# Kernel optimization log

Hardware: AMD Instinct MI355X
Metric: run time of the kernel (lower is better)

Reference implementation:

```python
import jax, jax.numpy as jnp
import numpy as np

# Model dims (scaled-down ModelArgs, ratios preserved)
B, L, Dm = 2, 1024, 1024
H, KVH = 16, 4
HD = Dm // H          # head_dim = 64
N = 64                # ssm_state_dim
E, TOPK = 4, 2        # num_experts, expert_top_k
FF = 4 * Dm           # expert hidden
ROUTER_MIX = np.array([0.5, 0.2, 0.15, 0.15], dtype=np.float32)  # layer_idx=0 -> ssm-heavy


def _rms(x, w, eps=1e-6):
    return x * jax.lax.rsqrt(jnp.mean(x * x, axis=-1, keepdims=True) + eps) * w


def setup_inputs() -> dict:
    key = jax.random.key(0)
    ks = jax.random.split(key, 32)
    f32 = jnp.float32
    def nrm(k, shape, s=0.02):
        return (s * jax.random.normal(k, shape)).astype(f32)
    inp = {
        'x': jax.random.normal(ks[0], (B, L, Dm), dtype=f32),
        'goal_cond': 0.1 * jax.random.normal(ks[1], (B, L, Dm), dtype=f32),
        'mem_out': jax.random.normal(ks[2], (B, L, Dm), dtype=f32),
        'norm1_w': jnp.ones((Dm,), f32),
        'norm2_w': jnp.ones((Dm,), f32),
        'router_w': nrm(ks[3], (Dm, 4)),
        'xproj_w': nrm(ks[4], (Dm, 2 * N + H)),
        'A': (-1.0 + 0.1 * jax.random.normal(ks[5], (H, N))).astype(f32),
        'Dp': jnp.ones((H,), f32),
        'gate_w': nrm(ks[6], (Dm, Dm)),
        'gate_b': jnp.zeros((Dm,), f32),
        'ssd_o_w': nrm(ks[7], (Dm, Dm)),
        'q_w': nrm(ks[8], (Dm, Dm)),
        'k_w': nrm(ks[9], (Dm, KVH * HD)),
        'v_w': nrm(ks[10], (Dm, KVH * HD)),
        'o_w': nrm(ks[11], (Dm, Dm)),
        'qn_w': jnp.ones((HD,), f32),
        'kn_w': jnp.ones((HD,), f32),
        'dw_w': nrm(ks[12], (Dm, 3), 0.3),
        'dw_b': jnp.zeros((Dm,), f32),
        'pw_w': nrm(ks[13], (Dm, Dm)),
        'pw_b': jnp.zeros((Dm,), f32),
        'moe_gate_w': nrm(ks[14], (Dm, E)),
        'e_w1': nrm(ks[15], (E, Dm, 2 * FF)),
        'e_w2': nrm(ks[16], (E, FF, Dm)),
        'e_lin_w': nrm(ks[17], (E, Dm, Dm)),
        'e_lin_b': jnp.zeros((E, Dm), f32),
    }
    return inp


def reference(x, goal_cond, mem_out, norm1_w, norm2_w, router_w, xproj_w, A, Dp,
              gate_w, gate_b, ssd_o_w, q_w, k_w, v_w, o_w, qn_w, kn_w,
              dw_w, dw_b, pw_w, pw_b, moe_gate_w, e_w1, e_w2, e_lin_w, e_lin_b):
    b, l, d = x.shape
    res = x
    xn = _rms(x, norm1_w) + goal_cond

    # --- router over 4 paths ---
    w = jax.nn.softmax(xn @ router_w, axis=-1) * jnp.asarray(ROUTER_MIX, x.dtype)
    w = w / w.sum(axis=-1, keepdims=True)  # [B,L,4]

    # --- SSD (Mamba-2 style selective scan) ---
    ssm = xn @ xproj_w                              # [B,L,2N+H]
    Bs, Cs, db = ssm[..., :N], ssm[..., N:2 * N], ssm[..., 2 * N:]
    delta = jax.nn.softplus(db[..., None] + Bs[..., None, :])   # [B,L,H,N]

    def step(s, dt):                                 # s,dt: [B,H,N]
        s = jnp.exp(dt * A) * s + dt * dt
        return s, s
    _, states = jax.lax.scan(step, jnp.zeros((b, H, N), x.dtype), jnp.moveaxis(delta, 1, 0))
    states = jnp.moveaxis(states, 0, 1)              # [B,L,H,N]
    y = jnp.einsum('blhn,bln->blh', states, Cs)      # contract state dim with C
    xg = xn.reshape(b, l, H, HD)
    y = (y[..., None] + xg * Dp[:, None]).reshape(b, l, d)
    gate = jax.nn.sigmoid(xn @ gate_w + gate_b)
    out_ssd = (y * gate) @ ssd_o_w

    # --- GQA attention with qk-norm + RoPE ---
    q = (xn @ q_w).reshape(b, l, H, HD).transpose(0, 2, 1, 3)      # [B,H,L,hd]
    k = (xn @ k_w).reshape(b, l, KVH, HD).transpose(0, 2, 1, 3)
    v = (xn @ v_w).reshape(b, l, KVH, HD).transpose(0, 2, 1, 3)
    q, k = _rms(q, qn_w), _rms(k, kn_w)
    inv_freq = 1.0 / (10000.0 ** (jnp.arange(0, HD, 2, dtype=jnp.float32) / HD))
    fr = jnp.arange(l, dtype=jnp.float32)[:, None] * inv_freq[None, :]
    emb = jnp.concatenate([fr, fr], axis=-1)
    cos, sin = jnp.cos(emb).astype(x.dtype), jnp.sin(emb).astype(x.dtype)
    def rot(u):
        u1, u2 = jnp.split(u, 2, axis=-1)
        return jnp.concatenate([-u2, u1], axis=-1)
    q = q * cos + rot(q) * sin
    k = k * cos + rot(k) * sin
    k = jnp.repeat(k, H // KVH, axis=1)
    v = jnp.repeat(v, H // KVH, axis=1)
    sc = jnp.einsum('bhqd,bhkd->bhqk', q, k) / jnp.sqrt(jnp.asarray(HD, x.dtype))
    attn = jnp.einsum('bhqk,bhkd->bhqd', jax.nn.softmax(sc, axis=-1), v)
    out_attn = attn.transpose(0, 2, 1, 3).reshape(b, l, d) @ o_w

    # --- depthwise conv3 -> silu -> pointwise conv1 ---
    xp = jnp.pad(xn, ((0, 0), (1, 1), (0, 0)))
    dw = xp[:, :-2] * dw_w[:, 0] + xp[:, 1:-1] * dw_w[:, 1] + xp[:, 2:] * dw_w[:, 2] + dw_b
    out_conv = jax.nn.silu(dw) @ pw_w + pw_b

    mixed = (w[..., 0:1] * out_ssd + w[..., 1:2] * out_attn +
             w[..., 2:3] * out_conv + w[..., 3:4] * mem_out)
    x2 = res + mixed

    # --- dense top-k MoE (experts applied over full x as in source) ---
    gp = jax.nn.softmax(_rms(x2, norm2_w) @ moe_gate_w, axis=-1)     # [B,L,E]
    topp, topi = jax.lax.top_k(gp, TOPK)
    wfull = (jax.nn.one_hot(topi, E, dtype=x.dtype) * topp[..., None]).sum(axis=-2)  # [B,L,E]
    moe = jnp.zeros_like(x2)
    for e in range(E):
        h = x2 @ e_w1[e]                     # [B,L,2*FF]
        a, g = jnp.split(h, 2, axis=-1)
        h = (jax.nn.silu(a) * g) @ e_w2[e]   # [B,L,D]
        eo = h @ e_lin_w[e] + e_lin_b[e]
        moe = moe + wfull[..., e:e + 1] * eo
    return x2 + moe
```

## Files before the change

### kernel.cpp

```cpp
#include <hip/hip_runtime.h>
#include <hip/hip_bf16.h>
#include <cstdint>

typedef unsigned short u16;
typedef __attribute__((ext_vector_type(4))) float f32x4;
typedef __attribute__((ext_vector_type(8))) short s16x8;

#define DEV __device__ __forceinline__

DEV u16 f2bf(float x) {
  unsigned u = __float_as_uint(x);
  u += 0x7FFFu + ((u >> 16) & 1u);
  return (u16)(u >> 16);
}
DEV float bf2f(u16 b) { return __uint_as_float(((unsigned)b) << 16); }

DEV void gload16(const void* g, void* l) {
  __builtin_amdgcn_global_load_lds(
      (const __attribute__((address_space(1))) void*)g,
      (__attribute__((address_space(3))) void*)l, 16, 0, 0);
}

template<bool MAXOP>
DEV float blockRed256(float v) {
  for (int o = 32; o; o >>= 1) {
    float t = __shfl_xor(v, o);
    v = MAXOP ? fmaxf(v, t) : v + t;
  }
  __shared__ float s[4];
  __syncthreads();
  if ((threadIdx.x & 63) == 0) s[threadIdx.x >> 6] = v;
  __syncthreads();
  return MAXOP ? fmaxf(fmaxf(s[0], s[1]), fmaxf(s[2], s[3]))
               : (s[0] + s[1] + s[2] + s[3]);
}

struct WtB { const float* in[8]; u16* out[8]; };
__global__ __launch_bounds__(256) void wtransb_k(WtB wb, int K, int N, int ilv) {
  const float* __restrict__ in = wb.in[blockIdx.z];
  u16* __restrict__ out = wb.out[blockIdx.z];
  __shared__ float t[64][68];
  const int n0 = blockIdx.x * 64, k0 = blockIdx.y * 64;
  const int tt = threadIdx.x;
  const int kl = tt >> 4, nl = (tt & 15) * 4;
#pragma unroll
  for (int i = 0; i < 4; ++i) {
    int k = kl + i * 16;
    float4 v{0.f, 0.f, 0.f, 0.f};
    if (n0 + nl + 3 < N) {
      v = *(const float4*)(in + (long long)(k0 + k) * N + n0 + nl);
    } else {
      for (int j = 0; j < 4; ++j)
        if (n0 + nl + j < N) ((float*)&v)[j] = in[(long long)(k0 + k) * N + n0 + nl + j];
    }
    t[nl + 0][k] = v.x; t[nl + 1][k] = v.y; t[nl + 2][k] = v.z; t[nl + 3][k] = v.w;
  }
  __syncthreads();
  const int n = tt >> 2, kq = (tt & 3) * 16;
  if (n0 + n < N) {
    s16x8 o0, o1;
#pragma unroll
    for (int j = 0; j < 8; ++j) { o0[j] = (short)f2bf(t[n][kq + j]); o1[j] = (short)f2bf(t[n][kq + 8 + j]); }
    int c = n0 + n;
    int r = ilv ? ((((c & 4095) >> 4) << 5) + ((c >> 12) << 4) + (c & 15)) : c;
    u16* op = out + (long long)r * K + k0 + kq;
    *(s16x8*)op = o0; *(s16x8*)(op + 8) = o1;
  }
}

struct GemmP {
  const u16* A; int lda; long long sAz;
  const u16* B; int ldb; long long sBz;
  void* C; int ldc; long long sCz;
  int M, N, K;
  int gqa;
  int czmode;
  const float *p0, *p1, *p2, *p3;
  float scale; int eidx;
  u16 *aux0, *aux1, *aux2;
  const int* cnt;
  const int* s2t;
  int xcdr;
};

template<int EPI, int TN>
__global__ __launch_bounds__(256) void gemm_k(GemmP p) {
  constexpr int NF = TN / 32;
  __shared__ u16 Al[2][128 * 64];
  __shared__ u16 Bl[2][TN * 64];
  __shared__ float sminv[128];
  int bx = blockIdx.x, by = blockIdx.y, z = blockIdx.z;
  if (p.xcdr) {
    const int nx = gridDim.x, ny = gridDim.y;
    const int chunk = nx >> 3;
    int flat = (blockIdx.z * ny + blockIdx.y) * nx + blockIdx.x;
    int c = flat & 7, i = flat >> 3;
    by = i % ny;
    int rest = i / ny;
    bx = c * chunk + rest % chunk;
    z = rest / chunk;
  }
  const int t = threadIdx.x;
  const int lane = t & 63, wid = t >> 6;
  const int wm = wid >> 1, wn = wid & 1;
  const int m0 = by * 128, n0 = bx * TN;
  if (p.cnt && m0 >= p.cnt[p.eidx + z]) return;
  const int* s2te = p.s2t ? p.s2t + (p.eidx + z) * 2048 : nullptr;

  const u16* Ab = p.A + (long long)z * p.sAz;
  const u16* Bb = p.B + (p.gqa ? (long long)(((z >> 4) << 2) + ((z & 15) >> 2)) * p.sBz
                               : (long long)z * p.sBz);
  const int sr = lane >> 3;
  const int sg = (lane & 7) ^ sr;
  long long pao[4]; int lao[4];
  long long pbo[NF]; int lbo[NF];
#pragma unroll
  for (int c = 0; c < 4; ++c) {
    int rbase = c * 32 + wid * 8;
    int ra = m0 + rbase + sr; if (ra > p.M - 1) ra = p.M - 1;
    if (s2te) ra = s2te[ra];
    pao[c] = (long long)ra * p.lda + sg * 8;
    lao[c] = rbase * 64;
  }
#pragma unroll
  for (int c = 0; c < NF; ++c) {
    int rbase = c * 32 + wid * 8;
    int rb = n0 + rbase + sr; if (rb > p.N - 1) rb = p.N - 1;
    pbo[c] = (long long)rb * p.ldb + sg * 8;
    lbo[c] = rbase * 64;
  }

  if (EPI == 11) {
    int r = t >> 1, h2 = t & 1;
    u16* rp = p.aux0 + (long long)z * p.sAz + (long long)(m0 + r) * 1024 + h2 * 8;
    float mx = -1e30f;
    for (int it = 0; it < 64; ++it) {
      s16x8 v = *(const s16x8*)(rp + it * 16);
#pragma unroll
      for (int q = 0; q < 8; ++q) mx = fmaxf(mx, bf2f((u16)v[q]));
    }
    mx = fmaxf(mx, __shfl_xor(mx, 1));
    float sum = 0.f;
    for (int it = 0; it < 64; ++it) {
      s16x8 v = *(s16x8*)(rp + it * 16);
      s16x8 o;
#pragma unroll
      for (int q = 0; q < 8; ++q) {
        float e = __expf(bf2f((u16)v[q]) - mx);
        sum += e;
        o[q] = (short)f2bf(e);
      }
      *(s16x8*)(rp + it * 16) = o;
    }
    sum += __shfl_xor(sum, 1);
    if (!h2) sminv[r] = 1.f / sum;
    asm volatile("s_waitcnt vmcnt(0)" ::: "memory");
    __syncthreads();
  }

  f32x4 acc[4][NF];
#pragma unroll
  for (int i = 0; i < 4; ++i)
#pragma unroll
    for (int j = 0; j < NF; ++j) acc[i][j] = f32x4{0.f, 0.f, 0.f, 0.f};

#pragma unroll
  for (int c = 0; c < 4; ++c) gload16(Ab + pao[c], &Al[0][lao[c]]);
#pragma unroll
  for (int c = 0; c < NF; ++c) gload16(Bb + pbo[c], &Bl[0][lbo[c]]);
  __syncthreads();

  const int lr = lane & 15, lk = lane >> 4;
  int cur = 0;
  for (int k0 = 0; k0 < p.K; k0 += 64) {
    int nxt = cur ^ 1;
    if (k0 + 64 < p.K) {
#pragma unroll
      for (int c = 0; c < 4; ++c) gload16(Ab + pao[c] + k0 + 64, &Al[nxt][lao[c]]);
#pragma unroll
      for (int c = 0; c < NF; ++c) gload16(Bb + pbo[c] + k0 + 64, &Bl[nxt][lbo[c]]);
    }
#pragma unroll
    for (int kk = 0; kk < 2; ++kk) {
      s16x8 af[4], bfr[NF];
      int g = kk * 4 + lk;
#pragma unroll
      for (int i = 0; i < 4; ++i) {
        int ra = wm * 64 + i * 16 + lr;
        af[i] = *(const s16x8*)&Al[cur][ra * 64 + ((g ^ (ra & 7)) * 8)];
      }
#pragma unroll
      for (int j = 0; j < NF; ++j) {
        int rb = wn * (TN / 2) + j * 16 + lr;
        bfr[j] = *(const s16x8*)&Bl[cur][rb * 64 + ((g ^ (rb & 7)) * 8)];
      }
#pragma unroll
      for (int i = 0; i < 4; ++i)
#pragma unroll
        for (int j = 0; j < NF; ++j)
          acc[i][j] = __builtin_amdgcn_mfma_f32_16x16x32_bf16(af[i], bfr[j], acc[i][j], 0, 0, 0);
    }
    __syncthreads();
    cur = nxt;
  }

  long long cb;
  if (p.czmode == 1) { int b = z >> 4, h = z & 15; cb = (long long)b * 1048576 + h * 64; }
  else cb = (long long)z * p.sCz;
  const int lq = lane >> 4;

  if (EPI == 8) {
#pragma unroll
    for (int i = 0; i < 4; ++i) {
#pragma unroll
      for (int u = 0; u < NF / 2; ++u) {
        int pcol = (n0 >> 1) + wn * (TN / 4) + u * 16 + lr;
#pragma unroll
        for (int q = 0; q < 4; ++q) {
          int row = m0 + wm * 64 + i * 16 + lq * 4 + q;
          float a = acc[i][2 * u][q], gg = acc[i][2 * u + 1][q];
          ((u16*)p.C)[cb + (long long)row * p.ldc + pcol] =
              f2bf(a / (1.f + __expf(-a)) * gg);
        }
      }
    }
    return;
  }
#pragma unroll
  for (int i = 0; i < 4; ++i) {
#pragma unroll
    for (int j = 0; j < NF; ++j) {
      int col = n0 + wn * (TN / 2) + j * 16 + lr;
      if (col >= p.N) continue;
#pragma unroll
      for (int q = 0; q < 4; ++q) {
        int row = m0 + wm * 64 + i * 16 + lq * 4 + q;
        float v = acc[i][j][q];
        if (EPI == 0) {
          ((u16*)p.C)[cb + (long long)row * p.ldc + col] = f2bf(v);
        } else if (EPI == 1) {
          ((float*)p.C)[cb + (long long)row * p.ldc + col] = v;
        } else if (EPI == 5) {
          ((u16*)p.C)[cb + (long long)row * p.ldc + col] = f2bf(v * p.scale);
        } else if (EPI == 9) {
          float add = (z == 2) ? p.p0[col] : 0.f;
          ((float*)p.C)[cb + (long long)row * p.ldc + col] = v + add;
        } else if (EPI == 11) {
          float sc = sminv[wm * 64 + i * 16 + lq * 4 + q];
          ((u16*)p.C)[cb + (long long)row * p.ldc + col] = f2bf(v * sc);
        } else if (EPI == 10) {
          if (col < 1024) {
            float gg = 1.f / (1.f + __expf(-(v + p.p0[col])));
            float yv = p.p1[row * 16 + (col >> 6)] +
                       p.p2[(long long)row * 1024 + col] * p.p3[col >> 6];
            ((u16*)p.C)[(long long)row * p.ldc + col] = f2bf(gg * yv);
          } else {
            int c2 = col - 1024;
            if (c2 < 1024) {
              p.aux0[(long long)row * 1024 + c2] = f2bf(v);
            } else if (c2 < 1280) {
              p.aux1[(long long)row * 256 + (c2 - 1024)] = f2bf(v);
            } else {
              int cc = c2 - 1280;
              int b = row >> 10, l = row & 1023, kvh = cc >> 6, d = cc & 63;
              p.aux2[(((long long)(b * 4 + kvh) * 64 + d) << 10) + l] = f2bf(v);
            }
          }
        }
      }
    }
  }
}

__global__ void rms1router_k(const float* x, const float* goal, const float* w,
                             const float* rw, float* xn, u16* xnb, float* wout) {
  int m = blockIdx.x, t = threadIdx.x;
  const float* xr = x + (long long)m * 1024;
  float v[4]; float ss = 0.f;
#pragma unroll
  for (int i = 0; i < 4; ++i) { v[i] = xr[t + i * 256]; ss += v[i] * v[i]; }
  ss = blockRed256<false>(ss);
  float r = rsqrtf(ss * (1.f / 1024.f) + 1e-6f);
  float a[4] = {0.f, 0.f, 0.f, 0.f};
#pragma unroll
  for (int i = 0; i < 4; ++i) {
    int c = t + i * 256;
    float o = v[i] * r * w[c] + goal[(long long)m * 1024 + c];
    xn[(long long)m * 1024 + c] = o;
    xnb[(long long)m * 1024 + c] = f2bf(o);
    const float* rr = rw + c * 4;
    a[0] += o * rr[0]; a[1] += o * rr[1]; a[2] += o * rr[2]; a[3] += o * rr[3];
  }
#pragma unroll
  for (int j = 0; j < 4; ++j) a[j] = blockRed256<false>(a[j]);
  if (t == 0) {
    float mx = fmaxf(fmaxf(a[0], a[1]), fmaxf(a[2], a[3]));
    float e[4]; float s = 0.f;
    for (int j = 0; j < 4; ++j) { e[j] = __expf(a[j] - mx); s += e[j]; }
    const float mix[4] = {0.5f, 0.2f, 0.15f, 0.15f};
    float ws = 0.f;
    for (int j = 0; j < 4; ++j) { e[j] = e[j] / s * mix[j]; ws += e[j]; }
    for (int j = 0; j < 4; ++j) wout[m * 4 + j] = e[j] / ws;
  }
}

DEV float softplus_f(float x) { return x > 15.f ? x : log1pf(__expf(x)); }

__global__ void scanA_k(const float* ssm, const float* A, float* aprod, float* sloc) {
  int blk = blockIdx.x, n = threadIdx.x;
  int c = blk & 63, h = (blk >> 6) & 15, b = blk >> 10;
  float Ah = A[h * 64 + n];
  float ap = 1.f, s = 0.f;
  int l0 = c * 16;
  for (int j = 0; j < 16; ++j) {
    long long off = (long long)(b * 1024 + l0 + j) * 144;
    float d = softplus_f(ssm[off + 128 + h] + ssm[off + n]);
    float a = __expf(d * Ah);
    s = a * s + d * d;
    ap *= a;
  }
  long long o = (long long)blk * 64 + n;
  aprod[o] = ap; sloc[o] = s;
}

__global__ void scanB_k(const float* aprod, const float* sloc, float* cin) {
  int bh = blockIdx.x, n = threadIdx.x;
  float carry = 0.f;
  for (int c = 0; c < 64; ++c) {
    long long o = (long long)(bh * 64 + c) * 64 + n;
    cin[o] = carry;
    carry = aprod[o] * carry + sloc[o];
  }
}

__global__ void scanC_k(const float* ssm, const float* A, const float* cin, float* ysm) {
  int blk = blockIdx.x, n = threadIdx.x;
  int c = blk & 63, h = (blk >> 6) & 15, b = blk >> 10;
  float Ah = A[h * 64 + n];
  float s = cin[(long long)blk * 64 + n];
  int l0 = c * 16;
  for (int j = 0; j < 16; ++j) {
    long long off = (long long)(b * 1024 + l0 + j) * 144;
    float d = softplus_f(ssm[off + 128 + h] + ssm[off + n]);
    float a = __expf(d * Ah);
    s = a * s + d * d;
    float yv = s * ssm[off + 64 + n];
    for (int o2 = 32; o2; o2 >>= 1) yv += __shfl_xor(yv, o2);
    if (n == 0) ysm[(long long)(b * 1024 + l0 + j) * 16 + h] = yv;
  }
}

__global__ void rtab_k(float2* rt) {
  int i = blockIdx.x * 256 + threadIdx.x;
  int l = i >> 5, f = i & 31;
  float fr = (float)l * powf(10000.f, -(float)f * (1.f / 32.f));
  rt[i] = float2{cosf(fr), sinf(fr)};
}

__global__ void rope_k(const u16* qpre, const u16* kpre, const float* qnw,
                       const float* knw, const float2* rtab, u16* qro, u16* kro) {
  int rid = blockIdx.x * 4 + (threadIdx.x >> 6);
  int lane = threadIdx.x & 63;
  float v; const float* nw; int l; u16* dst;
  if (rid < 32768) {
    int b = rid >> 14, h = (rid >> 10) & 15; l = rid & 1023;
    v = bf2f(qpre[(long long)(b * 1024 + l) * 1024 + h * 64 + lane]);
    nw = qnw; dst = qro + (long long)rid * 64;
  } else {
    int r2 = rid - 32768;
    int b = r2 >> 12, kvh = (r2 >> 10) & 3; l = r2 & 1023;
    v = bf2f(kpre[(long long)(b * 1024 + l) * 256 + kvh * 64 + lane]);
    nw = knw; dst = kro + (long long)r2 * 64;
  }
  float ss = v * v;
  for (int o = 32; o; o >>= 1) ss += __shfl_xor(ss, o);
  float r = rsqrtf(ss * (1.f / 64.f) + 1e-6f);
  float vn = v * r * nw[lane];
  float pt = __shfl_xor(vn, 32);
  float2 cs = rtab[l * 32 + (lane & 31)];
  float o2 = vn * cs.x + ((lane < 32) ? -pt : pt) * cs.y;
  dst[lane] = f2bf(o2);
}

__global__ void conv_k(const float* xn, const float* dww, const float* dwb, u16* outb) {
  int m = blockIdx.x; int l = m & 1023;
#pragma unroll
  for (int i = 0; i < 4; ++i) {
    int d = threadIdx.x + i * 256;
    float xm = l > 0    ? xn[(long long)(m - 1) * 1024 + d] : 0.f;
    float x0 =            xn[(long long)m * 1024 + d];
    float xp = l < 1023 ? xn[(long long)(m + 1) * 1024 + d] : 0.f;
    float dv = xm * dww[d * 3] + x0 * dww[d * 3 + 1] + xp * dww[d * 3 + 2] + dwb[d];
    outb[(long long)m * 1024 + d] = f2bf(dv / (1.f + __expf(-dv)));
  }
}

__global__ void mixmoegate_k(const float* x, const float* w, const float* o3,
                             const float* mem, const float* n2w, const float* mg,
                             float* x2, u16* x2b, float* wf) {
  int m = blockIdx.x, t = threadIdx.x;
  float w0 = w[m * 4], w1 = w[m * 4 + 1], w2 = w[m * 4 + 2], w3 = w[m * 4 + 3];
  float ss = 0.f, a[4] = {0.f, 0.f, 0.f, 0.f};
#pragma unroll
  for (int j = 0; j < 4; ++j) {
    int c = t + j * 256;
    long long i = (long long)m * 1024 + c;
    float v = x[i] + w0 * o3[i] + w1 * o3[i + 2097152] + w2 * o3[i + 4194304] +
              w3 * mem[i];
    x2[i] = v; x2b[i] = f2bf(v);
    ss += v * v;
    float vw = v * n2w[c];
    const float* g = mg + c * 4;
    a[0] += vw * g[0]; a[1] += vw * g[1]; a[2] += vw * g[2]; a[3] += vw * g[3];
  }
  ss = blockRed256<false>(ss);
#pragma unroll
  for (int j = 0; j < 4; ++j) a[j] = blockRed256<false>(a[j]);
  if (t == 0) {
    float r = rsqrtf(ss * (1.f / 1024.f) + 1e-6f);
    float mx = -1e30f;
    for (int j = 0; j < 4; ++j) { a[j] *= r; mx = fmaxf(mx, a[j]); }
    float e[4]; float s = 0.f;
    for (int j = 0; j < 4; ++j) { e[j] = __expf(a[j] - mx); s += e[j]; }
    for (int j = 0; j < 4; ++j) e[j] /= s;
    int i0 = 0;
    for (int j = 1; j < 4; ++j) if (e[j] > e[i0]) i0 = j;
    int i1 = -1;
    for (int j = 0; j < 4; ++j) { if (j == i0) continue; if (i1 < 0 || e[j] > e[i1]) i1 = j; }
    for (int j = 0; j < 4; ++j) wf[m * 4 + j] = (j == i0 || j == i1) ? e[j] : 0.f;
  }
}

__global__ void escan_k(const float* wf, int* cnt, int* s2t, int* t2s) {
  int e = threadIdx.x >> 6, lane = threadIdx.x & 63;
  int base = 0;
  for (int c = 0; c < 32; ++c) {
    int m = c * 64 + lane;
    bool r = wf[m * 4 + e] != 0.f;
    unsigned long long mask = __ballot(r);
    int pre = __popcll(mask & ((1ull << lane) - 1ull));
    if (r) { s2t[e * 2048 + base + pre] = m; t2s[m * 4 + e] = base + pre; }
    else t2s[m * 4 + e] = -1;
    base += __popcll(mask);
  }
  if (lane == 0) cnt[e] = base;
  for (int s = base + lane; s < 2048; s += 64) s2t[e * 2048 + s] = 0;
}

__global__ void final2_k(const float* x2, const float* wf, const int* t2s,
                         const float* t3, const float* elb, float* out) {
  int m = blockIdx.x, c4 = threadIdx.x * 4;
  long long i = (long long)m * 1024 + c4;
  float4 val = *(const float4*)(x2 + i);
#pragma unroll
  for (int e = 0; e < 4; ++e) {
    int s = t2s[m * 4 + e];
    if (s < 0) continue;
    float w = wf[m * 4 + e];
    float4 v = *(const float4*)(t3 + ((long long)e * 2048 + s) * 1024 + c4);
    float4 b = *(const float4*)(elb + e * 1024 + c4);
    val.x += w * (v.x + b.x); val.y += w * (v.y + b.y);
    val.z += w * (v.z + b.z); val.w += w * (v.w + b.w);
  }
  *(float4*)(out + i) = val;
}

extern "C" void kernel_launch(void* const* d_in, const int* in_sizes, int n_in,
                              void* d_out, int out_size, void* d_ws, size_t ws_size,
                              hipStream_t stream) {
  const float* x    = (const float*)d_in[0];
  const float* goal = (const float*)d_in[1];
  const float* mem  = (const float*)d_in[2];
  const float* n1w  = (const float*)d_in[3];
  const float* n2w  = (const float*)d_in[4];
  const float* rw   = (const float*)d_in[5];
  const float* xpw  = (const float*)d_in[6];
  const float* Amat = (const float*)d_in[7];
  const float* Dp   = (const float*)d_in[8];
  const float* gw   = (const float*)d_in[9];
  const float* gb   = (const float*)d_in[10];
  const float* sow  = (const float*)d_in[11];
  const float* qw   = (const float*)d_in[12];
  const float* kw   = (const float*)d_in[13];
  const float* vw   = (const float*)d_in[14];
  const float* ow   = (const float*)d_in[15];
  const float* qnw  = (const float*)d_in[16];
  const float* knw  = (const float*)d_in[17];
  const float* dww  = (const float*)d_in[18];
  const float* dwb  = (const float*)d_in[19];
  const float* pww  = (const float*)d_in[20];
  const float* pwb  = (const float*)d_in[21];
  const float* mgw  = (const float*)d_in[22];
  const float* ew1  = (const float*)d_in[23];
  const float* ew2  = (const float*)d_in[24];
  const float* elw  = (const float*)d_in[25];
  const float* elb  = (const float*)d_in[26];
  float* out = (float*)d_out;

  char* base = (char*)d_ws; size_t off = 0;
  auto alloc = [&](size_t b) { void* p = base + off; off += (b + 255) & ~(size_t)255; return p; };
  float* xn    = (float*)alloc(2048ull * 1024 * 4);
  u16*   xnb   = (u16*)  alloc(2048ull * 1024 * 2);
  float* wr    = (float*)alloc(2048ull * 4 * 4);
  float* ssm   = (float*)alloc(2048ull * 144 * 4);
  float* aprod = (float*)alloc(2048ull * 64 * 4);
  float* sloc  = (float*)alloc(2048ull * 64 * 4);
  float* cin   = (float*)alloc(2048ull * 64 * 4);
  float* ysm   = (float*)alloc(2048ull * 16 * 4);
  u16*   qpre  = (u16*)  alloc(2048ull * 1024 * 2);
  u16*   kpre  = (u16*)  alloc(2048ull * 256 * 2);
  u16*   vT    = (u16*)  alloc(2048ull * 256 * 2);
  u16*   qro   = (u16*)  alloc(2048ull * 1024 * 2);
  u16*   kro   = (u16*)  alloc(2048ull * 256 * 2);
  u16*   SA3   = (u16*)  alloc(3ull * 2048 * 1024 * 2);
  u16*   ssdin = SA3;
  u16*   acat  = SA3 + 2097152;
  u16*   cva   = SA3 + 4194304;
  float* t3    = (float*)base;
  float* x2    = (float*)alloc(2048ull * 1024 * 4);
  u16*   x2b   = (u16*)  alloc(2048ull * 1024 * 2);
  float* wfull = (float*)alloc(2048ull * 4 * 4);
  int*   ecnt  = (int*)  alloc(4 * 4);
  int*   s2t   = (int*)  alloc(4ull * 2048 * 4);
  int*   t2s   = (int*)  alloc(2048ull * 4 * 4);
  float2* rtab = (float2*)alloc(32768ull * 8);
  u16* xpwt  = (u16*)alloc(256ull  * 1024 * 2);
  u16* gqkvt = (u16*)alloc(2560ull * 1024 * 2);
  u16* w3t   = (u16*)alloc(3ull * 1024 * 1024 * 2);
  char*  U1    = (char*) alloc(25165824ull);
  float* outs3 = (float*)U1;
  u16*   t2_4  = (u16*)  U1;
  char* BIG = (char*)alloc(67108864ull);
  u16* scores = (u16*)BIG;
  u16* act4   = (u16*)BIG;
  char* EW = (char*)alloc(33554432ull);
  u16* ew1t  = (u16*)EW;
  u16* ew2t4 = (u16*)EW;
  u16* ewlt4 = (u16*)EW;

  rtab_k<<<128, 256, 0, stream>>>(rtab);
  { WtB wb{}; wb.in[0] = gw;  wb.out[0] = gqkvt;
    wb.in[1] = qw;  wb.out[1] = gqkvt + 1048576ull;
    wb.in[2] = sow; wb.out[2] = w3t;
    wb.in[3] = ow;  wb.out[3] = w3t + 1048576ull;
    wb.in[4] = pww; wb.out[4] = w3t + 2097152ull;
    wtransb_k<<<dim3(16, 16, 5), 256, 0, stream>>>(wb, 1024, 1024, 0); }
  { WtB wb{}; wb.in[0] = kw; wb.out[0] = gqkvt + 2097152ull;
    wb.in[1] = vw; wb.out[1] = gqkvt + 2359296ull;
    wtransb_k<<<dim3(4, 16, 2), 256, 0, stream>>>(wb, 1024, 256, 0); }
  { WtB wb{}; wb.in[0] = xpw; wb.out[0] = xpwt;
    wtransb_k<<<dim3(3, 16, 1), 256, 0, stream>>>(wb, 1024, 144, 0); }

  rms1router_k<<<2048, 256, 0, stream>>>(x, goal, n1w, rw, xn, xnb, wr);

  { GemmP p{}; p.A = xnb; p.lda = 1024; p.B = xpwt; p.ldb = 1024; p.C = ssm; p.ldc = 144;
    p.M = 2048; p.N = 144; p.K = 1024;
    gemm_k<1, 64><<<dim3(3, 16, 1), 256, 0, stream>>>(p); }

  scanA_k<<<2048, 64, 0, stream>>>(ssm, Amat, aprod, sloc);
  scanB_k<<<32, 64, 0, stream>>>(aprod, sloc, cin);
  scanC_k<<<2048, 64, 0, stream>>>(ssm, Amat, cin, ysm);

  { GemmP p{}; p.A = xnb; p.lda = 1024; p.B = gqkvt; p.ldb = 1024; p.C = ssdin; p.ldc = 1024;
    p.M = 2048; p.N = 2560; p.K = 1024; p.p0 = gb; p.p1 = ysm; p.p2 = xn; p.p3 = Dp;
    p.aux0 = qpre; p.aux1 = kpre; p.aux2 = vT;
    gemm_k<10, 64><<<dim3(40, 16, 1), 256, 0, stream>>>(p); }

  rope_k<<<10240, 256, 0, stream>>>(qpre, kpre, qnw, knw, rtab, qro, kro);

  { GemmP p{}; p.A = qro; p.lda = 64; p.sAz = 65536; p.B = kro; p.ldb = 64; p.sBz = 65536;
    p.gqa = 1; p.C = scores; p.ldc = 1024; p.sCz = 1048576;
    p.M = 1024; p.N = 1024; p.K = 64; p.scale = 0.125f;
    gemm_k<5, 128><<<dim3(8, 8, 32), 256, 0, stream>>>(p); }
  { GemmP p{}; p.A = scores; p.lda = 1024; p.sAz = 1048576; p.B = vT; p.ldb = 1024; p.sBz = 65536;
    p.gqa = 1; p.C = acat; p.ldc = 1024; p.czmode = 1; p.aux0 = scores;
    p.M = 1024; p.N = 64; p.K = 1024;
    gemm_k<11, 64><<<dim3(1, 8, 32), 256, 0, stream>>>(p); }

  conv_k<<<2048, 256, 0, stream>>>(xn, dww, dwb, cva);

  { GemmP p{}; p.A = SA3; p.lda = 1024; p.sAz = 2097152; p.B = w3t; p.ldb = 1024;
    p.sBz = 1048576; p.C = outs3; p.ldc = 1024; p.sCz = 2097152;
    p.M = 2048; p.N = 1024; p.K = 1024; p.p0 = pwb;
    gemm_k<9, 64><<<dim3(16, 16, 3), 256, 0, stream>>>(p); }

  mixmoegate_k<<<2048, 256, 0, stream>>>(x, wr, outs3, mem, n2w, mgw, x2, x2b, wfull);
  escan_k<<<1, 256, 0, stream>>>(wfull, ecnt, s2t, t2s);

  for (int pr = 0; pr < 2; ++pr) {
    int e0 = pr * 2;
    { WtB wb{}; wb.in[0] = ew1 + (long long)e0 * 8388608; wb.out[0] = ew1t;
      wb.in[1] = ew1 + (long long)(e0 + 1) * 8388608; wb.out[1] = ew1t + 8388608ull;
      wtransb_k<<<dim3(128, 16, 2), 256, 0, stream>>>(wb, 1024, 8192, 1); }
    GemmP p{}; p.A = x2b; p.lda = 1024; p.sAz = 0; p.B = ew1t; p.ldb = 1024; p.sBz = 8192ll * 1024;
    p.C = act4 + (long long)e0 * (2048ll * 4096); p.ldc = 4096; p.sCz = 2048ll * 4096;
    p.M = 2048; p.N = 8192; p.K = 1024; p.eidx = e0; p.cnt = ecnt; p.s2t = s2t; p.xcdr = 1;
    gemm_k<8, 64><<<dim3(128, 16, 2), 256, 0, stream>>>(p);
  }
  { WtB wb{};
    for (int e = 0; e < 4; ++e) {
      wb.in[e] = ew2 + (long long)e * 4194304;
      wb.out[e] = ew2t4 + (long long)e * (1024ll * 4096);
    }
    wtransb_k<<<dim3(16, 64, 4), 256, 0, stream>>>(wb, 4096, 1024, 0); }
  { GemmP p{}; p.A = act4; p.lda = 4096; p.sAz = 2048ll * 4096; p.B = ew2t4; p.ldb = 4096;
    p.sBz = 1024ll * 4096; p.C = t2_4; p.ldc = 1024; p.sCz = 2048ll * 1024;
    p.M = 2048; p.N = 1024; p.K = 4096; p.cnt = ecnt; p.xcdr = 1;
    gemm_k<0, 64><<<dim3(16, 16, 4), 256, 0, stream>>>(p); }
  { WtB wb{};
    for (int e = 0; e < 4; ++e) {
      wb.in[e] = elw + (long long)e * 1048576;
      wb.out[e] = ewlt4 + (long long)e * (1024ll * 1024);
    }
    wtransb_k<<<dim3(16, 16, 4), 256, 0, stream>>>(wb, 1024, 1024, 0); }
  { GemmP p{}; p.A = t2_4; p.lda = 1024; p.sAz = 2048ll * 1024; p.B = ewlt4; p.ldb = 1024;
    p.sBz = 1024ll * 1024; p.C = t3; p.ldc = 1024; p.sCz = 2048ll * 1024;
    p.M = 2048; p.N = 1024; p.K = 1024; p.cnt = ecnt; p.xcdr = 1;
    gemm_k<1, 64><<<dim3(16, 16, 4), 256, 0, stream>>>(p); }

  final2_k<<<2048, 256, 0, stream>>>(x2, wfull, t2s, t3, elb, out);
}
```

Before: 563.6 us.

## Add triple-buffered LDS pipeline with MFMA priority boost to MoE GEMMs

Adds a PIPE template option to the GEMM kernel that keeps three LDS stages instead of two. Loads run two K-tiles ahead, with a partial vmcnt wait, a raw s_barrier in place of __syncthreads, and s_setprio raised around the MFMA block. The aim is to hide global-load latency better in the three MoE expert GEMMs. In exchange it uses more shared memory, which may lower occupancy, and the hand-set vmcnt(6) relies on an exact count of outstanding loads per thread (4 A + NF B loads).

```diff
diff --git a/kernel.cpp b/kernel.cpp
--- a/kernel.cpp
+++ b/kernel.cpp
@@ -83,11 +83,12 @@
   int xcdr;
 };
 
-template<int EPI, int TN>
+template<int EPI, int TN, int PIPE = 0>
 __global__ __launch_bounds__(256) void gemm_k(GemmP p) {
   constexpr int NF = TN / 32;
-  __shared__ u16 Al[2][128 * 64];
-  __shared__ u16 Bl[2][TN * 64];
+  constexpr int NB = PIPE ? 3 : 2;
+  __shared__ u16 Al[NB][128 * 64];
+  __shared__ u16 Bl[NB][TN * 64];
   __shared__ float sminv[128];
   int bx = blockIdx.x, by = blockIdx.y, z = blockIdx.z;
   if (p.xcdr) {
@@ -164,44 +165,99 @@
 #pragma unroll
     for (int j = 0; j < NF; ++j) acc[i][j] = f32x4{0.f, 0.f, 0.f, 0.f};
 
-#pragma unroll
-  for (int c = 0; c < 4; ++c) gload16(Ab + pao[c], &Al[0][lao[c]]);
-#pragma unroll
-  for (int c = 0; c < NF; ++c) gload16(Bb + pbo[c], &Bl[0][lbo[c]]);
-  __syncthreads();
-
   const int lr = lane & 15, lk = lane >> 4;
-  int cur = 0;
-  for (int k0 = 0; k0 < p.K; k0 += 64) {
-    int nxt = cur ^ 1;
-    if (k0 + 64 < p.K) {
-#pragma unroll
-      for (int c = 0; c < 4; ++c) gload16(Ab + pao[c] + k0 + 64, &Al[nxt][lao[c]]);
-#pragma unroll
-      for (int c = 0; c < NF; ++c) gload16(Bb + pbo[c] + k0 + 64, &Bl[nxt][lbo[c]]);
-    }
-#pragma unroll
-    for (int kk = 0; kk < 2; ++kk) {
-      s16x8 af[4], bfr[NF];
-      int g = kk * 4 + lk;
-#pragma unroll
-      for (int i = 0; i < 4; ++i) {
-        int ra = wm * 64 + i * 16 + lr;
-        af[i] = *(const s16x8*)&Al[cur][ra * 64 + ((g ^ (ra & 7)) * 8)];
+
+  if constexpr (PIPE) {
+    const int NT = p.K >> 6;
+#pragma unroll
+    for (int c = 0; c < 4; ++c) gload16(Ab + pao[c], &Al[0][lao[c]]);
+#pragma unroll
+    for (int c = 0; c < NF; ++c) gload16(Bb + pbo[c], &Bl[0][lbo[c]]);
+    if (NT > 1) {
+#pragma unroll
+      for (int c = 0; c < 4; ++c) gload16(Ab + pao[c] + 64, &Al[1][lao[c]]);
+#pragma unroll
+      for (int c = 0; c < NF; ++c) gload16(Bb + pbo[c] + 64, &Bl[1][lbo[c]]);
+    }
+    asm volatile("s_waitcnt vmcnt(6)" ::: "memory");
+    __builtin_amdgcn_s_barrier();
+    int cur = 0, stg = 2;
+    for (int ts = 0; ts < NT; ++ts) {
+      if (ts + 2 < NT) {
+        long long ko = (long long)(ts + 2) * 64;
+#pragma unroll
+        for (int c = 0; c < 4; ++c) gload16(Ab + pao[c] + ko, &Al[stg][lao[c]]);
+#pragma unroll
+        for (int c = 0; c < NF; ++c) gload16(Bb + pbo[c] + ko, &Bl[stg][lbo[c]]);
+        asm volatile("s_waitcnt vmcnt(6)" ::: "memory");
+      } else {
+        asm volatile("s_waitcnt vmcnt(0)" ::: "memory");
       }
 #pragma unroll
-      for (int j = 0; j < NF; ++j) {
-        int rb = wn * (TN / 2) + j * 16 + lr;
-        bfr[j] = *(const s16x8*)&Bl[cur][rb * 64 + ((g ^ (rb & 7)) * 8)];
+      for (int kk = 0; kk < 2; ++kk) {
+        s16x8 af[4], bfr[NF];
+        int g = kk * 4 + lk;
+#pragma unroll
+        for (int i = 0; i < 4; ++i) {
+          int ra = wm * 64 + i * 16 + lr;
+          af[i] = *(const s16x8*)&Al[cur][ra * 64 + ((g ^ (ra & 7)) * 8)];
+        }
+#pragma unroll
+        for (int j = 0; j < NF; ++j) {
+          int rb = wn * (TN / 2) + j * 16 + lr;
+          bfr[j] = *(const s16x8*)&Bl[cur][rb * 64 + ((g ^ (rb & 7)) * 8)];
+        }
+        __builtin_amdgcn_s_setprio(1);
+#pragma unroll
+        for (int i = 0; i < 4; ++i)
+#pragma unroll
+          for (int j = 0; j < NF; ++j)
+            acc[i][j] = __builtin_amdgcn_mfma_f32_16x16x32_bf16(af[i], bfr[j], acc[i][j], 0, 0, 0);
+        __builtin_amdgcn_s_setprio(0);
       }
-#pragma unroll
-      for (int i = 0; i < 4; ++i)
-#pragma unroll
-        for (int j = 0; j < NF; ++j)
-          acc[i][j] = __builtin_amdgcn_mfma_f32_16x16x32_bf16(af[i], bfr[j], acc[i][j], 0, 0, 0);
-    }
+      asm volatile("s_waitcnt lgkmcnt(0)" ::: "memory");
+      __builtin_amdgcn_s_barrier();
+      cur = (cur + 1 == 3) ? 0 : cur + 1;
+      stg = (stg + 1 == 3) ? 0 : stg + 1;
+    }
+  } else {
+#pragma unroll
+    for (int c = 0; c < 4; ++c) gload16(Ab + pao[c], &Al[0][lao[c]]);
+#pragma unroll
+    for (int c = 0; c < NF; ++c) gload16(Bb + pbo[c], &Bl[0][lbo[c]]);
     __syncthreads();
-    cur = nxt;
+    int cur = 0;
+    for (int k0 = 0; k0 < p.K; k0 += 64) {
+      int nxt = cur ^ 1;
+      if (k0 + 64 < p.K) {
+#pragma unroll
+        for (int c = 0; c < 4; ++c) gload16(Ab + pao[c] + k0 + 64, &Al[nxt][lao[c]]);
+#pragma unroll
+        for (int c = 0; c < NF; ++c) gload16(Bb + pbo[c] + k0 + 64, &Bl[nxt][lbo[c]]);
+      }
+#pragma unroll
+      for (int kk = 0; kk < 2; ++kk) {
+        s16x8 af[4], bfr[NF];
+        int g = kk * 4 + lk;
+#pragma unroll
+        for (int i = 0; i < 4; ++i) {
+          int ra = wm * 64 + i * 16 + lr;
+          af[i] = *(const s16x8*)&Al[cur][ra * 64 + ((g ^ (ra & 7)) * 8)];
+        }
+#pragma unroll
+        for (int j = 0; j < NF; ++j) {
+          int rb = wn * (TN / 2) + j * 16 + lr;
+          bfr[j] = *(const s16x8*)&Bl[cur][rb * 64 + ((g ^ (rb & 7)) * 8)];
+        }
+#pragma unroll
+        for (int i = 0; i < 4; ++i)
+#pragma unroll
+          for (int j = 0; j < NF; ++j)
+            acc[i][j] = __builtin_amdgcn_mfma_f32_16x16x32_bf16(af[i], bfr[j], acc[i][j], 0, 0, 0);
+      }
+      __syncthreads();
+      cur = nxt;
+    }
   }
 
   long long cb;
@@ -595,7 +651,7 @@
     GemmP p{}; p.A = x2b; p.lda = 1024; p.sAz = 0; p.B = ew1t; p.ldb = 1024; p.sBz = 8192ll * 1024;
     p.C = act4 + (long long)e0 * (2048ll * 4096); p.ldc = 4096; p.sCz = 2048ll * 4096;
     p.M = 2048; p.N = 8192; p.K = 1024; p.eidx = e0; p.cnt = ecnt; p.s2t = s2t; p.xcdr = 1;
-    gemm_k<8, 64><<<dim3(128, 16, 2), 256, 0, stream>>>(p);
+    gemm_k<8, 64, 1><<<dim3(128, 16, 2), 256, 0, stream>>>(p);
   }
   { WtB wb{};
     for (int e = 0; e < 4; ++e) {
@@ -606,7 +662,7 @@
   { GemmP p{}; p.A = act4; p.lda = 4096; p.sAz = 2048ll * 4096; p.B = ew2t4; p.ldb = 4096;
     p.sBz = 1024ll * 4096; p.C = t2_4; p.ldc = 1024; p.sCz = 2048ll * 1024;
     p.M = 2048; p.N = 1024; p.K = 4096; p.cnt = ecnt; p.xcdr = 1;
-    gemm_k<0, 64><<<dim3(16, 16, 4), 256, 0, stream>>>(p); }
+    gemm_k<0, 64, 1><<<dim3(16, 16, 4), 256, 0, stream>>>(p); }
   { WtB wb{};
     for (int e = 0; e < 4; ++e) {
       wb.in[e] = elw + (long long)e * 1048576;
@@ -616,7 +672,7 @@
   { GemmP p{}; p.A = t2_4; p.lda = 1024; p.sAz = 2048ll * 1024; p.B = ewlt4; p.ldb = 1024;
     p.sBz = 1024ll * 1024; p.C = t3; p.ldc = 1024; p.sCz = 2048ll * 1024;
     p.M = 2048; p.N = 1024; p.K = 1024; p.cnt = ecnt; p.xcdr = 1;
-    gemm_k<1, 64><<<dim3(16, 16, 4), 256, 0, stream>>>(p); }
+    gemm_k<1, 64, 1><<<dim3(16, 16, 4), 256, 0, stream>>>(p); }
 
   final2_k<<<2048, 256, 0, stream>>>(x2, wfull, t2s, t3, elb, out);
 }
```

New measurement: 648.2 us. +15.0%, slower.
